# Kernel tuning notes

Measured on AMD Instinct MI355X. Metric: run time of the kernel, lower is better.

## Reference

```python
import jax, jax.numpy as jnp
import numpy as np

N_NODES = 50000
N_EDGES = 800000
NUM_GRAPHS = 256
EPS = 1e-5


def _gcn_conv(x, edge_index, W, b):
    # PyG GCNConv: add self-loops, sym-normalize, aggregate, then add bias.
    n = x.shape[0]
    xw = x @ W  # [N, out]
    loops = jnp.arange(n)
    row = jnp.concatenate([edge_index[0], loops])  # source
    col = jnp.concatenate([edge_index[1], loops])  # target
    deg = jax.ops.segment_sum(jnp.ones_like(col, dtype=xw.dtype), col, num_segments=n)
    dinv = jnp.where(deg > 0, jax.lax.rsqrt(deg), 0.0)
    norm = dinv[row] * dinv[col]  # [E+N]
    msg = norm[:, None] * xw[row]  # gather + scale
    out = jax.ops.segment_sum(msg, col, num_segments=n)  # scatter-add
    return out + b


def _bn(x, g, b, m, v):
    # inference-mode batch norm
    return (x - m) * jax.lax.rsqrt(v + EPS) * g + b


def reference(x, edge_index, batch, gcn_W0, gcn_b0, bn_g0, bn_b0, bn_m0, bn_v0,
              gcn_W1, gcn_b1, bn_g1, bn_b1, bn_m1, bn_v1,
              hW1, hb1, hg1, hbb1, hm1, hv1,
              hW2, hb2, hg2, hbb2, hm2, hv2,
              hW3, hb3, hW4, hb4):
    # GCN block 0
    h = _gcn_conv(x, edge_index, gcn_W0, gcn_b0)
    h = jax.nn.relu(_bn(h, bn_g0, bn_b0, bn_m0, bn_v0))  # dropout = identity (eval)
    # GCN block 1
    h = _gcn_conv(h, edge_index, gcn_W1, gcn_b1)
    h = jax.nn.relu(_bn(h, bn_g1, bn_b1, bn_m1, bn_v1))
    # global mean pool over graphs
    sums = jax.ops.segment_sum(h, batch, num_segments=NUM_GRAPHS)
    cnts = jax.ops.segment_sum(jnp.ones_like(batch, dtype=h.dtype), batch, num_segments=NUM_GRAPHS)
    pooled = sums / jnp.maximum(cnts, 1.0)[:, None]  # [G, 64]
    # MLP head (eval: dropout identity)
    z = jax.nn.relu(_bn(pooled @ hW1 + hb1, hg1, hbb1, hm1, hv1))
    z = jax.nn.relu(_bn(z @ hW2 + hb2, hg2, hbb2, hm2, hv2))
    z = jax.nn.relu(z @ hW3 + hb3)
    out = (z @ hW4 + hb4).reshape(-1)  # [G]
    return out


def setup_inputs() -> dict:
    key = jax.random.key(0)
    ks = jax.random.split(key, 12)
    d = 64
    inp = {
        'x': jax.random.normal(ks[0], (N_NODES, d), dtype=jnp.float32),
        'edge_index': jax.random.randint(ks[1], (2, N_EDGES), 0, N_NODES, dtype=jnp.int64),
        'batch': jnp.sort(jax.random.randint(ks[2], (N_NODES,), 0, NUM_GRAPHS, dtype=jnp.int64)),
        'gcn_W0': jax.random.normal(ks[3], (d, d), dtype=jnp.float32) * 0.1,
        'gcn_b0': jnp.zeros((d,), jnp.float32),
        'bn_g0': jnp.ones((d,), jnp.float32), 'bn_b0': jnp.zeros((d,), jnp.float32),
        'bn_m0': jnp.zeros((d,), jnp.float32), 'bn_v0': jnp.ones((d,), jnp.float32),
        'gcn_W1': jax.random.normal(ks[4], (d, d), dtype=jnp.float32) * 0.1,
        'gcn_b1': jnp.zeros((d,), jnp.float32),
        'bn_g1': jnp.ones((d,), jnp.float32), 'bn_b1': jnp.zeros((d,), jnp.float32),
        'bn_m1': jnp.zeros((d,), jnp.float32), 'bn_v1': jnp.ones((d,), jnp.float32),
        'hW1': jax.random.normal(ks[5], (d, 256), dtype=jnp.float32) * 0.1,
        'hb1': jnp.zeros((256,), jnp.float32),
        'hg1': jnp.ones((256,), jnp.float32), 'hbb1': jnp.zeros((256,), jnp.float32),
        'hm1': jnp.zeros((256,), jnp.float32), 'hv1': jnp.ones((256,), jnp.float32),
        'hW2': jax.random.normal(ks[6], (256, 128), dtype=jnp.float32) * 0.1,
        'hb2': jnp.zeros((128,), jnp.float32),
        'hg2': jnp.ones((128,), jnp.float32), 'hbb2': jnp.zeros((128,), jnp.float32),
        'hm2': jnp.zeros((128,), jnp.float32), 'hv2': jnp.ones((128,), jnp.float32),
        'hW3': jax.random.normal(ks[7], (128, 64), dtype=jnp.float32) * 0.1,
        'hb3': jnp.zeros((64,), jnp.float32),
        'hW4': jax.random.normal(ks[8], (64, 1), dtype=jnp.float32) * 0.1,
        'hb4': jnp.zeros((1,), jnp.float32),
    }
    return inp
```

## Files before the change

### kernel.cpp

```cpp
#include <hip/hip_runtime.h>
#include <hip/hip_bf16.h>
#include <hip/hip_fp16.h>

#define N_NODES 50000
#define N_EDGES 800000
#define NUM_GRAPHS 256
#define D 64
#define EPS 1e-5f
#define N_PART 8
#define PART_SIZE (N_NODES / N_PART)
#define SCAT_CHUNKS 512

__global__ __launch_bounds__(256) void scatter_cnt_kernel(
        const int* __restrict__ ei, int* __restrict__ cnt,
        int* __restrict__ ssrc, int cap, int E) {
    int p     = blockIdx.x & (N_PART - 1);
    int chunk = blockIdx.x >> 3;
    int per   = (E + SCAT_CHUNKS - 1) / SCAT_CHUNKS;
    int lo    = chunk * per;
    int hi    = lo + per; if (hi > E) hi = E;
    for (int e = lo + threadIdx.x; e < hi; e += 256) {
        int c = ei[E + e];
        if (c / PART_SIZE == p) {
            int r = ei[e];
            int pos = atomicAdd(&cnt[c], 1);
            if (pos < cap) ssrc[(size_t)c * cap + pos] = r;
        }
    }
}

__global__ __launch_bounds__(256) void gemm64_kernel(const float* __restrict__ X,
                                                     const float* __restrict__ W,
                                                     __half* __restrict__ Yh, int N) {
    __shared__ float Ws[64 * 64];
    __shared__ float Xs[64 * 65];
    int base = blockIdx.x * 64;
    for (int i = threadIdx.x; i < 1024; i += 256)
        ((float4*)Ws)[i] = ((const float4*)W)[i];
    for (int i = threadIdx.x; i < 1024; i += 256) {
        int rr = i >> 4, cc = (i & 15) * 4;
        float4 xv = (base + rr < N)
            ? ((const float4*)X)[(size_t)(base + rr) * 16 + (i & 15)]
            : make_float4(0.f, 0.f, 0.f, 0.f);
        float* dst = &Xs[rr * 65 + cc];
        dst[0] = xv.x; dst[1] = xv.y; dst[2] = xv.z; dst[3] = xv.w;
    }
    __syncthreads();
    int rg = (threadIdx.x >> 4) * 4;
    int cg = (threadIdx.x & 15) * 4;
    float4 a0 = make_float4(0.f,0.f,0.f,0.f);
    float4 a1 = a0, a2 = a0, a3 = a0;
#pragma unroll
    for (int k = 0; k < 64; k++) {
        float4 wv = *(const float4*)&Ws[k * 64 + cg];
        float x0 = Xs[(rg + 0) * 65 + k];
        float x1 = Xs[(rg + 1) * 65 + k];
        float x2 = Xs[(rg + 2) * 65 + k];
        float x3 = Xs[(rg + 3) * 65 + k];
        a0.x += x0*wv.x; a0.y += x0*wv.y; a0.z += x0*wv.z; a0.w += x0*wv.w;
        a1.x += x1*wv.x; a1.y += x1*wv.y; a1.z += x1*wv.z; a1.w += x1*wv.w;
        a2.x += x2*wv.x; a2.y += x2*wv.y; a2.z += x2*wv.z; a2.w += x2*wv.w;
        a3.x += x3*wv.x; a3.y += x3*wv.y; a3.z += x3*wv.z; a3.w += x3*wv.w;
    }
#pragma unroll
    for (int j = 0; j < 4; j++) {
        float4 a = (j == 0) ? a0 : (j == 1) ? a1 : (j == 2) ? a2 : a3;
        int row = base + rg + j;
        if (row < N) {
            __half2 p0 = __floats2half2_rn(a.x, a.y);
            __half2 p1 = __floats2half2_rn(a.z, a.w);
            uint2 v;
            v.x = *(unsigned int*)&p0;
            v.y = *(unsigned int*)&p1;
            *((uint2*)&Yh[(size_t)row * 64 + cg]) = v;
        }
    }
}

__global__ __launch_bounds__(256) void agg_bn_kernel(
        const __half* __restrict__ xwh, const int* __restrict__ cnt,
        const int* __restrict__ ssrc, int cap,
        const float* __restrict__ b, const float* __restrict__ g,
        const float* __restrict__ bb, const float* __restrict__ m,
        const float* __restrict__ var,
        float* __restrict__ out, int N) {
    int wave = (blockIdx.x * blockDim.x + threadIdx.x) >> 6;
    int lane = threadIdx.x & 63;
    if (wave >= N) return;
    int c   = wave;
    int sub = lane >> 3;
    int f2  = lane & 7;
    const uint4* xw8 = (const uint4*)xwh;
    int n = cnt[c];
    if (n > cap) n = cap;
    size_t base = (size_t)c * cap;
    float dc = rsqrtf((float)n + 1.0f);
    float4 accA = make_float4(0.f, 0.f, 0.f, 0.f);
    float4 accB = accA;
    if (sub == 0) {
        uint4 v = xw8[(size_t)c * 8 + f2];
        __half2* hp = (__half2*)&v;
        float2 q0 = __half22float2(hp[0]), q1 = __half22float2(hp[1]);
        float2 q2 = __half22float2(hp[2]), q3 = __half22float2(hp[3]);
        accA.x = dc * q0.x; accA.y = dc * q0.y; accA.z = dc * q1.x; accA.w = dc * q1.y;
        accB.x = dc * q2.x; accB.y = dc * q2.y; accB.z = dc * q3.x; accB.w = dc * q3.y;
    }
    for (int e0 = 0; e0 < n; e0 += 8) {
        int e = e0 + sub;
        if (e < n) {
            int   r = ssrc[base + e];
            float w = rsqrtf((float)cnt[r] + 1.0f);
            uint4 v = xw8[(size_t)r * 8 + f2];
            __half2* hp = (__half2*)&v;
            float2 q0 = __half22float2(hp[0]), q1 = __half22float2(hp[1]);
            float2 q2 = __half22float2(hp[2]), q3 = __half22float2(hp[3]);
            accA.x += w * q0.x; accA.y += w * q0.y;
            accA.z += w * q1.x; accA.w += w * q1.y;
            accB.x += w * q2.x; accB.y += w * q2.y;
            accB.z += w * q3.x; accB.w += w * q3.y;
        }
    }
#pragma unroll
    for (int off = 8; off < 64; off <<= 1) {
        accA.x += __shfl_xor(accA.x, off, 64); accA.y += __shfl_xor(accA.y, off, 64);
        accA.z += __shfl_xor(accA.z, off, 64); accA.w += __shfl_xor(accA.w, off, 64);
        accB.x += __shfl_xor(accB.x, off, 64); accB.y += __shfl_xor(accB.y, off, 64);
        accB.z += __shfl_xor(accB.z, off, 64); accB.w += __shfl_xor(accB.w, off, 64);
    }
    if (sub == 0) {
        const float4* b4v  = (const float4*)b;
        const float4* m4v  = (const float4*)m;
        const float4* v4v  = (const float4*)var;
        const float4* g4v  = (const float4*)g;
        const float4* bb4v = (const float4*)bb;
#pragma unroll
        for (int half = 0; half < 2; half++) {
            int i4 = 2 * f2 + half;
            float4 acc = half ? accB : accA;
            float4 b4 = b4v[i4], m4 = m4v[i4], v4 = v4v[i4], g4 = g4v[i4], bb4 = bb4v[i4];
            float4 h;
            h.x = (acc.x * dc + b4.x - m4.x) * (1.0f / sqrtf(v4.x + EPS)) * g4.x + bb4.x;
            h.y = (acc.y * dc + b4.y - m4.y) * (1.0f / sqrtf(v4.y + EPS)) * g4.y + bb4.y;
            h.z = (acc.z * dc + b4.z - m4.z) * (1.0f / sqrtf(v4.z + EPS)) * g4.z + bb4.z;
            h.w = (acc.w * dc + b4.w - m4.w) * (1.0f / sqrtf(v4.w + EPS)) * g4.w + bb4.w;
            h.x = h.x > 0.f ? h.x : 0.f;
            h.y = h.y > 0.f ? h.y : 0.f;
            h.z = h.z > 0.f ? h.z : 0.f;
            h.w = h.w > 0.f ? h.w : 0.f;
            ((float4*)out)[(size_t)c * 16 + i4] = h;
        }
    }
}

__global__ __launch_bounds__(256) void pool_head_kernel(
        const float* __restrict__ h, const int* __restrict__ batch,
        const float* __restrict__ hW1, const float* __restrict__ hb1,
        const float* __restrict__ hg1, const float* __restrict__ hbb1,
        const float* __restrict__ hm1, const float* __restrict__ hv1,
        const float* __restrict__ hW2, const float* __restrict__ hb2,
        const float* __restrict__ hg2, const float* __restrict__ hbb2,
        const float* __restrict__ hm2, const float* __restrict__ hv2,
        const float* __restrict__ hW3, const float* __restrict__ hb3,
        const float* __restrict__ hW4, const float* __restrict__ hb4,
        float* __restrict__ out) {
    __shared__ int se[2];
    __shared__ float red[256];
    __shared__ float pooled[64];
    __shared__ float z1[256];
    __shared__ float z2[128];
    __shared__ float z3[64];
    int g = blockIdx.x;
    int t = threadIdx.x;
    if (t < 2) {
        int target = g + t;
        int lo = 0, hi = N_NODES;
        while (lo < hi) {
            int mid = (lo + hi) >> 1;
            if (batch[mid] < target) lo = mid + 1; else hi = mid;
        }
        se[t] = lo;
    }
    __syncthreads();
    int start = se[0], end = se[1];
    {
        int f = t & 63, rg = t >> 6;
        float part = 0.0f;
        for (int r = start + rg; r < end; r += 4) part += h[(size_t)r * 64 + f];
        red[t] = part;
        __syncthreads();
        if (t < 64) {
            float s = red[t] + red[t + 64] + red[t + 128] + red[t + 192];
            float cnt = (float)(end - start);
            cnt = cnt > 1.0f ? cnt : 1.0f;
            pooled[t] = s / cnt;
        }
    }
    __syncthreads();
    {
        float acc = hb1[t];
#pragma unroll
        for (int k = 0; k < 64; k++) acc += pooled[k] * hW1[k * 256 + t];
        acc = (acc - hm1[t]) * (1.0f / sqrtf(hv1[t] + EPS)) * hg1[t] + hbb1[t];
        z1[t] = acc > 0.0f ? acc : 0.0f;
    }
    __syncthreads();
    if (t < 128) {
        float acc = hb2[t];
#pragma unroll 8
        for (int k = 0; k < 256; k++) acc += z1[k] * hW2[k * 128 + t];
        acc = (acc - hm2[t]) * (1.0f / sqrtf(hv2[t] + EPS)) * hg2[t] + hbb2[t];
        z2[t] = acc > 0.0f ? acc : 0.0f;
    }
    __syncthreads();
    if (t < 64) {
        float acc = hb3[t];
#pragma unroll 8
        for (int k = 0; k < 128; k++) acc += z2[k] * hW3[k * 64 + t];
        z3[t] = acc > 0.0f ? acc : 0.0f;
    }
    __syncthreads();
    if (t < 64) {
        float v = z3[t] * hW4[t];
        for (int off = 32; off > 0; off >>= 1) v += __shfl_down(v, off, 64);
        if (t == 0) out[g] = v + hb4[0];
    }
}

extern "C" void kernel_launch(void* const* d_in, const int* in_sizes, int n_in,
                              void* d_out, int out_size, void* d_ws, size_t ws_size,
                              hipStream_t stream) {
    const float* x     = (const float*)d_in[0];
    const int*   ei    = (const int*)d_in[1];
    const int*   batch = (const int*)d_in[2];
    const float* W0 = (const float*)d_in[3];
    const float* b0 = (const float*)d_in[4];
    const float* g0 = (const float*)d_in[5];
    const float* bb0 = (const float*)d_in[6];
    const float* m0 = (const float*)d_in[7];
    const float* v0 = (const float*)d_in[8];
    const float* W1 = (const float*)d_in[9];
    const float* b1 = (const float*)d_in[10];
    const float* g1 = (const float*)d_in[11];
    const float* bb1 = (const float*)d_in[12];
    const float* m1 = (const float*)d_in[13];
    const float* v1 = (const float*)d_in[14];
    const float* hW1 = (const float*)d_in[15];
    const float* hb1 = (const float*)d_in[16];
    const float* hg1 = (const float*)d_in[17];
    const float* hbb1 = (const float*)d_in[18];
    const float* hm1 = (const float*)d_in[19];
    const float* hv1 = (const float*)d_in[20];
    const float* hW2 = (const float*)d_in[21];
    const float* hb2 = (const float*)d_in[22];
    const float* hg2 = (const float*)d_in[23];
    const float* hbb2 = (const float*)d_in[24];
    const float* hm2 = (const float*)d_in[25];
    const float* hv2 = (const float*)d_in[26];
    const float* hW3 = (const float*)d_in[27];
    const float* hb3 = (const float*)d_in[28];
    const float* hW4 = (const float*)d_in[29];
    const float* hb4 = (const float*)d_in[30];
    float* out = (float*)d_out;

    float*  bufA = (float*)d_ws;
    __half* xwh  = (__half*)bufA;
    float*  bufB = bufA + (size_t)N_NODES * D;
    int*    cnt  = (int*)(bufB + (size_t)N_NODES * D);
    int*    ssrc = cnt + N_NODES;

    size_t used  = ((size_t)2 * N_NODES * D + N_NODES) * 4;
    int cap = 64;
    if (ws_size >= used) {
        size_t avail = (ws_size - used) / ((size_t)N_NODES * 4);
        if (avail < (size_t)cap) cap = (int)avail & ~3;
    } else {
        cap = 0;
    }

    const int NT = 256;
    hipMemsetAsync(cnt, 0, (size_t)N_NODES * 4, stream);

    scatter_cnt_kernel<<<SCAT_CHUNKS * N_PART, NT, 0, stream>>>(ei, cnt, ssrc, cap, N_EDGES);

    gemm64_kernel<<<(N_NODES + 63) / 64, NT, 0, stream>>>(x, W0, xwh, N_NODES);
    agg_bn_kernel<<<(N_NODES * 64 + NT - 1) / NT, NT, 0, stream>>>(
        xwh, cnt, ssrc, cap, b0, g0, bb0, m0, v0, bufB, N_NODES);

    gemm64_kernel<<<(N_NODES + 63) / 64, NT, 0, stream>>>(bufB, W1, xwh, N_NODES);
    agg_bn_kernel<<<(N_NODES * 64 + NT - 1) / NT, NT, 0, stream>>>(
        xwh, cnt, ssrc, cap, b1, g1, bb1, m1, v1, bufB, N_NODES);

    pool_head_kernel<<<NUM_GRAPHS, NT, 0, stream>>>(bufB, batch,
        hW1, hb1, hg1, hbb1, hm1, hv1,
        hW2, hb2, hg2, hbb2, hm2, hv2,
        hW3, hb3, hW4, hb4, out);
}
```

Measured before the change: 319.9 us.

## Prescale GEMM output by source degree norm and store edge sources as uint16

```diff
diff --git a/kernel.cpp b/kernel.cpp
--- a/kernel.cpp
+++ b/kernel.cpp
@@ -13,7 +13,7 @@
 
 __global__ __launch_bounds__(256) void scatter_cnt_kernel(
         const int* __restrict__ ei, int* __restrict__ cnt,
-        int* __restrict__ ssrc, int cap, int E) {
+        unsigned short* __restrict__ ssrc, int cap, int E) {
     int p     = blockIdx.x & (N_PART - 1);
     int chunk = blockIdx.x >> 3;
     int per   = (E + SCAT_CHUNKS - 1) / SCAT_CHUNKS;
@@ -24,13 +24,14 @@
         if (c / PART_SIZE == p) {
             int r = ei[e];
             int pos = atomicAdd(&cnt[c], 1);
-            if (pos < cap) ssrc[(size_t)c * cap + pos] = r;
+            if (pos < cap) ssrc[(size_t)c * cap + pos] = (unsigned short)r;
         }
     }
 }
 
 __global__ __launch_bounds__(256) void gemm64_kernel(const float* __restrict__ X,
                                                      const float* __restrict__ W,
+                                                     const int* __restrict__ cnt,
                                                      __half* __restrict__ Yh, int N) {
     __shared__ float Ws[64 * 64];
     __shared__ float Xs[64 * 65];
@@ -67,8 +68,9 @@
         float4 a = (j == 0) ? a0 : (j == 1) ? a1 : (j == 2) ? a2 : a3;
         int row = base + rg + j;
         if (row < N) {
-            __half2 p0 = __floats2half2_rn(a.x, a.y);
-            __half2 p1 = __floats2half2_rn(a.z, a.w);
+            float ws = rsqrtf((float)cnt[row] + 1.0f);
+            __half2 p0 = __floats2half2_rn(ws * a.x, ws * a.y);
+            __half2 p1 = __floats2half2_rn(ws * a.z, ws * a.w);
             uint2 v;
             v.x = *(unsigned int*)&p0;
             v.y = *(unsigned int*)&p1;
@@ -79,7 +81,7 @@
 
 __global__ __launch_bounds__(256) void agg_bn_kernel(
         const __half* __restrict__ xwh, const int* __restrict__ cnt,
-        const int* __restrict__ ssrc, int cap,
+        const unsigned short* __restrict__ ssrc, int cap,
         const float* __restrict__ b, const float* __restrict__ g,
         const float* __restrict__ bb, const float* __restrict__ m,
         const float* __restrict__ var,
@@ -102,22 +104,21 @@
         __half2* hp = (__half2*)&v;
         float2 q0 = __half22float2(hp[0]), q1 = __half22float2(hp[1]);
         float2 q2 = __half22float2(hp[2]), q3 = __half22float2(hp[3]);
-        accA.x = dc * q0.x; accA.y = dc * q0.y; accA.z = dc * q1.x; accA.w = dc * q1.y;
-        accB.x = dc * q2.x; accB.y = dc * q2.y; accB.z = dc * q3.x; accB.w = dc * q3.y;
+        accA.x = q0.x; accA.y = q0.y; accA.z = q1.x; accA.w = q1.y;
+        accB.x = q2.x; accB.y = q2.y; accB.z = q3.x; accB.w = q3.y;
     }
     for (int e0 = 0; e0 < n; e0 += 8) {
         int e = e0 + sub;
         if (e < n) {
-            int   r = ssrc[base + e];
-            float w = rsqrtf((float)cnt[r] + 1.0f);
+            int r = (int)ssrc[base + e];
             uint4 v = xw8[(size_t)r * 8 + f2];
             __half2* hp = (__half2*)&v;
             float2 q0 = __half22float2(hp[0]), q1 = __half22float2(hp[1]);
             float2 q2 = __half22float2(hp[2]), q3 = __half22float2(hp[3]);
-            accA.x += w * q0.x; accA.y += w * q0.y;
-            accA.z += w * q1.x; accA.w += w * q1.y;
-            accB.x += w * q2.x; accB.y += w * q2.y;
-            accB.z += w * q3.x; accB.w += w * q3.y;
+            accA.x += q0.x; accA.y += q0.y;
+            accA.z += q1.x; accA.w += q1.y;
+            accB.x += q2.x; accB.y += q2.y;
+            accB.z += q3.x; accB.w += q3.y;
         }
     }
 #pragma unroll
@@ -266,12 +267,12 @@
     __half* xwh  = (__half*)bufA;
     float*  bufB = bufA + (size_t)N_NODES * D;
     int*    cnt  = (int*)(bufB + (size_t)N_NODES * D);
-    int*    ssrc = cnt + N_NODES;
+    unsigned short* ssrc = (unsigned short*)(cnt + N_NODES);
 
     size_t used  = ((size_t)2 * N_NODES * D + N_NODES) * 4;
     int cap = 64;
     if (ws_size >= used) {
-        size_t avail = (ws_size - used) / ((size_t)N_NODES * 4);
+        size_t avail = (ws_size - used) / ((size_t)N_NODES * 2);
         if (avail < (size_t)cap) cap = (int)avail & ~3;
     } else {
         cap = 0;
@@ -282,11 +283,11 @@
 
     scatter_cnt_kernel<<<SCAT_CHUNKS * N_PART, NT, 0, stream>>>(ei, cnt, ssrc, cap, N_EDGES);
 
-    gemm64_kernel<<<(N_NODES + 63) / 64, NT, 0, stream>>>(x, W0, xwh, N_NODES);
+    gemm64_kernel<<<(N_NODES + 63) / 64, NT, 0, stream>>>(x, W0, cnt, xwh, N_NODES);
     agg_bn_kernel<<<(N_NODES * 64 + NT - 1) / NT, NT, 0, stream>>>(
         xwh, cnt, ssrc, cap, b0, g0, bb0, m0, v0, bufB, N_NODES);
 
-    gemm64_kernel<<<(N_NODES + 63) / 64, NT, 0, stream>>>(bufB, W1, xwh, N_NODES);
+    gemm64_kernel<<<(N_NODES + 63) / 64, NT, 0, stream>>>(bufB, W1, cnt, xwh, N_NODES);
     agg_bn_kernel<<<(N_NODES * 64 + NT - 1) / NT, NT, 0, stream>>>(
         xwh, cnt, ssrc, cap, b1, g1, bb1, m1, v1, bufB, N_NODES);
 
```

Measured after the change: 323.7 us. No clear change (+1.2%).
